# Kernel tuning notes

Measured on AMD Instinct MI355X. Metric: run time of the kernel, lower is better.

## Reference

```python
import jax, jax.numpy as jnp
import numpy as np
from jax.scipy.special import logsumexp

N_PROBLEMS = 10000
N_KCS = 100
N_STATES = 2
N_OUTPUTS = 2
BATCH = 1024
T = 500
TAU = 1.5


def setup_inputs() -> dict:
    key = jax.random.key(0)
    k1, k2, k3, k4, k5, k6, k7, k8 = jax.random.split(key, 8)
    corr = jax.random.randint(k1, (BATCH, T), 0, N_OUTPUTS)
    kc = jax.random.randint(k2, (BATCH, T), 0, N_PROBLEMS)
    problem = jax.random.randint(k3, (BATCH, T), 0, N_PROBLEMS)
    # learned parameters (per MultiHmmCell.__init__)
    trans_logits = jax.random.normal(k4, (N_KCS, N_STATES, N_STATES), dtype=jnp.float32)
    obs_logits_problem = 0.1 * jax.random.normal(k5, (N_PROBLEMS, N_STATES, N_OUTPUTS), dtype=jnp.float32)
    init_logits = jax.random.normal(k6, (N_KCS, N_STATES), dtype=jnp.float32)
    # BktModel.sample_A: gumbel-softmax over kc_membership_logits (soft, tau=1.5)
    kc_membership_logits = jax.random.normal(k7, (N_PROBLEMS, N_KCS), dtype=jnp.float32)
    u = jax.random.uniform(k8, (N_PROBLEMS, N_KCS), minval=1e-6, maxval=1.0 - 1e-6)
    gumbel = -jnp.log(-jnp.log(u))
    A = jax.nn.softmax((kc_membership_logits + gumbel) / TAU, axis=1)
    return {"corr": corr, "kc": kc, "problem": problem, "A": A,
            "trans_logits": trans_logits, "obs_logits_problem": obs_logits_problem,
            "init_logits": init_logits}


def _hmm_forward(corr, kc, problem, A, trans_logits, obs_logits_problem, init_logits):
    n_batch = corr.shape[0]
    chain = A[kc]                                           # [B, T, K] soft KC membership
    log_t = jax.nn.log_softmax(trans_logits, axis=1)        # [K, S, S] (normalized over dim 1, as in torch)
    log_alpha0 = jnp.broadcast_to(jax.nn.log_softmax(init_logits, axis=1)[None],
                                  (n_batch, init_logits.shape[0], init_logits.shape[1]))  # [B, K, S]

    def step(log_alpha, x):
        chain_t, prob_t, obs_t = x                          # [B,K], [B], [B]
        log_obs = jax.nn.log_softmax(obs_logits_problem[prob_t], axis=2)  # [B, S, O]
        # predicted output distribution
        a1 = log_obs * jnp.sum(chain_t, axis=1)[:, None, None]            # [B, S, O]
        a2 = jnp.einsum('bk,bks->bs', chain_t, log_alpha)                 # [B, S]
        log_py = logsumexp(a1 + a2[:, :, None], axis=1)                   # [B, O]
        log_py = log_py - logsumexp(log_py, axis=1, keepdims=True)
        # alpha update given observed output
        obs_ll = jnp.take_along_axis(log_obs, obs_t[:, None, None], axis=2)[:, :, 0]  # [B, S]
        obs_ll = obs_ll * jnp.sum(chain_t, axis=1)[:, None]
        a1b = jnp.einsum('bks,bk->bs', log_alpha, chain_t)                # [B, S]
        a2b = jnp.einsum('kso,bk->bso', log_t, chain_t)                   # [B, S, S]
        a3 = logsumexp(obs_ll[:, None, :] + a1b[:, None, :] + a2b, axis=2)  # [B, S]
        new_alpha = (1.0 - chain_t[:, :, None]) * log_alpha + chain_t[:, :, None] * a3[:, None, :]
        return new_alpha, log_py

    xs = (jnp.swapaxes(chain, 0, 1), problem.T, corr.T)
    _, outs = jax.lax.scan(step, log_alpha0, xs)            # outs: [T, B, O]
    return jnp.swapaxes(outs, 0, 1)                         # [B, T, O]


def reference(corr, kc, problem, A, trans_logits, obs_logits_problem, init_logits):
    return _hmm_forward(corr, kc, problem, A, trans_logits, obs_logits_problem, init_logits)
```

## Files before the change

### kernel.cpp

```cpp
#include <hip/hip_runtime.h>
#include <math.h>

#define B_  1024
#define T_  500
#define K_  100
#define NP_ 10000
#define CH  32
#define NCH 16

__device__ __forceinline__ float lse2(float a, float b) {
    float m = fmaxf(a, b);
    return m + __logf(__expf(a - m) + __expf(b - m));
}

template<int CTRL, int RM>
__device__ __forceinline__ float dpp_add(float v) {
    int x = __builtin_amdgcn_update_dpp(0, __float_as_int(v), CTRL, RM, 0xf, true);
    return v + __int_as_float(x);
}

__device__ __forceinline__ float wave_sum(float v) {
    v = dpp_add<0x111, 0xf>(v);
    v = dpp_add<0x112, 0xf>(v);
    v = dpp_add<0x114, 0xf>(v);
    v = dpp_add<0x118, 0xf>(v);
    v = dpp_add<0x142, 0xa>(v);
    v = dpp_add<0x143, 0xc>(v);
    return __int_as_float(__builtin_amdgcn_readlane(__float_as_int(v), 63));
}

#define GLOAD16(gp, lp) __builtin_amdgcn_global_load_lds( \
    (const __attribute__((address_space(1))) unsigned int*)(gp), \
    (__attribute__((address_space(3))) unsigned int*)(lp), 16, 0, 0)
#define GLOAD4(gp, lp) __builtin_amdgcn_global_load_lds( \
    (const __attribute__((address_space(1))) unsigned int*)(gp), \
    (__attribute__((address_space(3))) unsigned int*)(lp), 4, 0, 0)
#define WAITV0 asm volatile("s_waitcnt vmcnt(0)" ::: "memory")

__global__ __launch_bounds__(64, 4) void bkt_pre(
    const float* __restrict__ A, const float* __restrict__ trans,
    const float* __restrict__ obs, float* __restrict__ Qtab,
    float* __restrict__ Stab, float* __restrict__ LOtab)
{
    const int p = blockIdx.x;
    const int lane = threadIdx.x;
    const int k0 = lane, k1 = lane + 64;
    const bool has1 = (k1 < K_);
    const int k1c = has1 ? k1 : k0;
    const float m1 = has1 ? 1.f : 0.f;

    float4 t0 = *reinterpret_cast<const float4*>(trans + k0 * 4);
    float l00 = lse2(t0.x, t0.z), l01 = lse2(t0.y, t0.w);
    float lt000 = t0.x - l00, lt001 = t0.y - l01;
    float lt010 = t0.z - l00, lt011 = t0.w - l01;
    float4 t1 = *reinterpret_cast<const float4*>(trans + k1c * 4);
    float l10 = lse2(t1.x, t1.z), l11 = lse2(t1.y, t1.w);
    float lt100 = t1.x - l10, lt101 = t1.y - l11;
    float lt110 = t1.z - l10, lt111 = t1.w - l11;

    const float* ar = A + (size_t)p * K_;
    float c0 = ar[k0];
    float c1 = ar[k1c] * m1;

    float sc  = wave_sum(c0 + c1);
    float q00 = wave_sum(c0 * lt000 + c1 * lt100);
    float q01 = wave_sum(c0 * lt001 + c1 * lt101);
    float q10 = wave_sum(c0 * lt010 + c1 * lt110);
    float q11 = wave_sum(c0 * lt011 + c1 * lt111);

    float4 ob = *reinterpret_cast<const float4*>(obs + (size_t)p * 4);
    float l0 = lse2(ob.x, ob.y), l1 = lse2(ob.z, ob.w);

    if (lane == 0) {
        reinterpret_cast<float4*>(Qtab)[p] = make_float4(q00, q01, q10, q11);
        Stab[p] = sc;
        reinterpret_cast<float4*>(LOtab)[p] =
            make_float4(ob.x - l0, ob.y - l0, ob.z - l1, ob.w - l1);
    }
}

__global__ __launch_bounds__(64, 1) void bkt_main(
    const int* __restrict__ corr, const int* __restrict__ kc,
    const int* __restrict__ problem, const float* __restrict__ A,
    const float* __restrict__ init, const float* __restrict__ Qtab,
    const float* __restrict__ Stab, const float* __restrict__ LOtab,
    float* __restrict__ out)
{
    const int b = blockIdx.x;
    const int lane = threadIdx.x;
    const int k1 = lane + 64;
    const bool has1 = (k1 < K_);
    const int k1c = has1 ? k1 : lane;
    const float m1 = has1 ? 1.f : 0.f;

    __shared__ float  s_c[2][CH * K_];
    __shared__ float4 s_ql[2][2 * CH];
    __shared__ float  s_s[2][CH];
    __shared__ int    s_kcpr[3][2 * CH];
    __shared__ int    s_y[3][CH];
    __shared__ float2 s_a2[CH];

    const int* kcb = kc + (size_t)b * T_;
    const int* prb = problem + (size_t)b * T_;
    const int* cob = corr + (size_t)b * T_;
    float* outp = out + (size_t)b * T_ * 2;

    float al00, al01, al10 = 0.f, al11 = 0.f;
    {
        float2 x = *reinterpret_cast<const float2*>(init + lane * 2);
        float l = lse2(x.x, x.y);
        al00 = x.x - l; al01 = x.y - l;
    }
    {
        float2 x = *reinterpret_cast<const float2*>(init + k1c * 2);
        float l = lse2(x.x, x.y);
        al10 = (x.x - l) * m1; al11 = (x.y - l) * m1;
    }

#define STAGEIDX(cn, ib) {                                                \
        int tt_ = (cn) * CH + (lane & 31);                                \
        tt_ = tt_ < T_ ? tt_ : T_ - 1;                                    \
        const int* is_ = (lane < 32 ? kcb : prb) + tt_;                   \
        GLOAD4(is_, &s_kcpr[ib][0]);                                      \
        if (lane < 32) GLOAD4(cob + tt_, &s_y[ib][0]);                    \
    }

#define GATHER(ib, db) {                                                  \
        int myidx_ = s_kcpr[ib][lane];                                    \
        const float* qlsrc_ = (lane < 32)                                 \
            ? (Qtab  + (size_t)myidx_ * 4)                                \
            : (LOtab + (size_t)myidx_ * 4);                               \
        GLOAD16(qlsrc_, &s_ql[db][0]);                                    \
        if (lane < 32) GLOAD4(Stab + myidx_, &s_s[db][0]);                \
        _Pragma("unroll")                                                 \
        for (int j_ = 0; j_ < 13; ++j_) {                                 \
            int f_ = j_ * 64 + lane;                                      \
            unsigned tf_ = ((unsigned)f_ * 5243u) >> 17;        \
            int q_ = f_ - (int)tf_ * 25;                                  \
            int kcv_ = s_kcpr[ib][tf_];                                   \
            const float* asrc_ = A + (size_t)kcv_ * K_ + q_ * 4;          \
            if (f_ < CH * 25) GLOAD16(asrc_, &s_c[db][j_ * 256]);         \
        }                                                                 \
    }

    STAGEIDX(0, 0);
    STAGEIDX(1, 1);
    WAITV0;
    GATHER(0, 0);

#pragma unroll 1
    for (int n = 0; n < NCH; ++n) {
        WAITV0;
        { int i2 = (n + 2) % 3; STAGEIDX(n + 2, i2); }
        { int i1 = (n + 1) % 3, d1 = (n + 1) & 1; GATHER(i1, d1); }

        const float*  cbuf = s_c[n & 1];
        const float4* qlb  = s_ql[n & 1];
        const float*  sb   = s_s[n & 1];
        const int*    yb   = s_y[n % 3];
        const int base = n * CH;

        float ca0 = cbuf[lane];
        float ca1 = cbuf[k1c] * m1;
        float a20 = wave_sum(ca0 * al00 + ca1 * al10);
        float a21 = wave_sum(ca0 * al01 + ca1 * al11);

#pragma unroll 2
        for (int u = 0; u < CH - 1; ++u) {
            float cb0 = cbuf[(u + 1) * K_ + lane];
            float cb1 = cbuf[(u + 1) * K_ + k1c] * m1;
            float4 Q = qlb[u];
            float4 L = qlb[CH + u];
            float  S = sb[u];
            int    y = yb[u];
            if (lane == 0) s_a2[u] = make_float2(a20, a21);
            float hs0 = ((y == 0) ? L.x : L.y) * S;
            float hs1 = ((y == 0) ? L.z : L.w) * S;
            float a30 = lse2(hs0 + Q.x + a20, hs1 + Q.y + a21);
            float a31 = lse2(hs0 + Q.z + a20, hs1 + Q.w + a21);
            float tu0 = cb0 * (1.f - ca0), tu1 = cb1 * (1.f - ca1);
            float U0 = wave_sum(tu0 * al00 + tu1 * al10);
            float U1 = wave_sum(tu0 * al01 + tu1 * al11);
            float Wv = wave_sum(cb0 * ca0 + cb1 * ca1);
            al00 += ca0 * (a30 - al00);
            al01 += ca0 * (a31 - al01);
            al10 += ca1 * (a30 - al10);
            al11 += ca1 * (a31 - al11);
            a20 = U0 + Wv * a30;
            a21 = U1 + Wv * a31;
            ca0 = cb0; ca1 = cb1;
        }
        {
            const int u = CH - 1;
            float4 Q = qlb[u];
            float4 L = qlb[CH + u];
            float  S = sb[u];
            int    y = yb[u];
            if (lane == 0) s_a2[u] = make_float2(a20, a21);
            float hs0 = ((y == 0) ? L.x : L.y) * S;
            float hs1 = ((y == 0) ? L.z : L.w) * S;
            float a30 = lse2(hs0 + Q.x + a20, hs1 + Q.y + a21);
            float a31 = lse2(hs0 + Q.z + a20, hs1 + Q.w + a21);
            al00 += ca0 * (a30 - al00);
            al01 += ca0 * (a31 - al01);
            al10 += ca1 * (a30 - al10);
            al11 += ca1 * (a31 - al11);
        }
        if (lane < 32) {
            float2 a2v = s_a2[lane];
            float4 L = qlb[CH + lane];
            float  S = sb[lane];
            float h00 = L.x * S, h01 = L.y * S, h10 = L.z * S, h11 = L.w * S;
            float py0 = lse2(h00 + a2v.x, h10 + a2v.y);
            float py1 = lse2(h01 + a2v.x, h11 + a2v.y);
            float nrm = lse2(py0, py1);
            int t = base + lane;
            if (t < T_)
                *reinterpret_cast<float2*>(outp + (size_t)t * 2) =
                    make_float2(py0 - nrm, py1 - nrm);
        }
    }
#undef STAGEIDX
#undef GATHER
}

extern "C" void kernel_launch(void* const* d_in, const int* in_sizes, int n_in,
                              void* d_out, int out_size, void* d_ws, size_t ws_size,
                              hipStream_t stream) {
    const int*   corr    = (const int*)d_in[0];
    const int*   kc      = (const int*)d_in[1];
    const int*   problem = (const int*)d_in[2];
    const float* A       = (const float*)d_in[3];
    const float* trans   = (const float*)d_in[4];
    const float* obs     = (const float*)d_in[5];
    const float* init    = (const float*)d_in[6];
    float* out = (float*)d_out;

    float* Qtab  = (float*)d_ws;
    float* LOtab = Qtab + (size_t)NP_ * 4;
    float* Stab  = LOtab + (size_t)NP_ * 4;

    bkt_pre<<<NP_, 64, 0, stream>>>(A, trans, obs, Qtab, Stab, LOtab);
    bkt_main<<<B_, 64, 0, stream>>>(corr, kc, problem, A, init, Qtab, Stab, LOtab, out);
}
```

Before: 251.0 us.

## Precompute chunk-local alpha projections to shorten the serial recurrence chain

Restructures the per-timestep recurrence so that all wave reductions that do not depend on the serial a3 values are computed up front for a chunk of 8 steps. These are the pairwise coupling coefficients P[t][j] and the initial-alpha projections. The serial loop then needs only scalar FMAs and lse2 per step instead of three wave reductions. The cost is more total reductions (O(CH^2) per chunk), heavy register use for the P matrix, and smaller chunks with more pipeline iterations.

```diff
diff --git a/kernel.cpp b/kernel.cpp
--- a/kernel.cpp
+++ b/kernel.cpp
@@ -5,8 +5,8 @@
 #define T_  500
 #define K_  100
 #define NP_ 10000
-#define CH  32
-#define NCH 16
+#define CH  8
+#define NCH 64
 
 __device__ __forceinline__ float lse2(float a, float b) {
     float m = fmaxf(a, b);
@@ -96,9 +96,7 @@
     __shared__ float  s_c[2][CH * K_];
     __shared__ float4 s_ql[2][2 * CH];
     __shared__ float  s_s[2][CH];
-    __shared__ int    s_kcpr[3][2 * CH];
-    __shared__ int    s_y[3][CH];
-    __shared__ float2 s_a2[CH];
+    __shared__ int    s_idx[3][3 * CH];
 
     const int* kcb = kc + (size_t)b * T_;
     const int* prb = problem + (size_t)b * T_;
@@ -118,28 +116,27 @@
     }
 
 #define STAGEIDX(cn, ib) {                                                \
-        int tt_ = (cn) * CH + (lane & 31);                                \
+        int tt_ = (cn) * CH + (lane & 7);                                 \
         tt_ = tt_ < T_ ? tt_ : T_ - 1;                                    \
-        const int* is_ = (lane < 32 ? kcb : prb) + tt_;                   \
-        GLOAD4(is_, &s_kcpr[ib][0]);                                      \
-        if (lane < 32) GLOAD4(cob + tt_, &s_y[ib][0]);                    \
+        const int* src_ = (lane < 8) ? (kcb + tt_)                        \
+                        : (lane < 16) ? (prb + tt_) : (cob + tt_);        \
+        if (lane < 24) GLOAD4(src_, &s_idx[ib][0]);                       \
     }
 
 #define GATHER(ib, db) {                                                  \
-        int myidx_ = s_kcpr[ib][lane];                                    \
-        const float* qlsrc_ = (lane < 32)                                 \
-            ? (Qtab  + (size_t)myidx_ * 4)                                \
-            : (LOtab + (size_t)myidx_ * 4);                               \
-        GLOAD16(qlsrc_, &s_ql[db][0]);                                    \
-        if (lane < 32) GLOAD4(Stab + myidx_, &s_s[db][0]);                \
+        int id_ = s_idx[ib][lane & 15];                                   \
+        const float* qls_ = (lane < 8) ? (Qtab + (size_t)id_ * 4)         \
+                                       : (LOtab + (size_t)id_ * 4);       \
+        if (lane < 16) GLOAD16(qls_, &s_ql[db][0]);                       \
+        if (lane < 8)  GLOAD4(Stab + id_, &s_s[db][0]);                   \
         _Pragma("unroll")                                                 \
-        for (int j_ = 0; j_ < 13; ++j_) {                                 \
+        for (int j_ = 0; j_ < 4; ++j_) {                                  \
             int f_ = j_ * 64 + lane;                                      \
             unsigned tf_ = ((unsigned)f_ * 5243u) >> 17;        \
             int q_ = f_ - (int)tf_ * 25;                                  \
-            int kcv_ = s_kcpr[ib][tf_];                                   \
-            const float* asrc_ = A + (size_t)kcv_ * K_ + q_ * 4;          \
-            if (f_ < CH * 25) GLOAD16(asrc_, &s_c[db][j_ * 256]);         \
+            int kcv_ = s_idx[ib][tf_];                                    \
+            if (f_ < CH * 25)                                             \
+                GLOAD16(A + (size_t)kcv_ * K_ + q_ * 4, &s_c[db][j_ * 256]); \
         }                                                                 \
     }
 
@@ -151,70 +148,89 @@
 #pragma unroll 1
     for (int n = 0; n < NCH; ++n) {
         WAITV0;
-        { int i2 = (n + 2) % 3; STAGEIDX(n + 2, i2); }
-        { int i1 = (n + 1) % 3, d1 = (n + 1) & 1; GATHER(i1, d1); }
+        STAGEIDX(n + 2, (n + 2) % 3);
+        GATHER((n + 1) % 3, (n + 1) & 1);
 
         const float*  cbuf = s_c[n & 1];
         const float4* qlb  = s_ql[n & 1];
         const float*  sb   = s_s[n & 1];
-        const int*    yb   = s_y[n % 3];
-        const int base = n * CH;
-
-        float ca0 = cbuf[lane];
-        float ca1 = cbuf[k1c] * m1;
-        float a20 = wave_sum(ca0 * al00 + ca1 * al10);
-        float a21 = wave_sum(ca0 * al01 + ca1 * al11);
-
-#pragma unroll 2
-        for (int u = 0; u < CH - 1; ++u) {
-            float cb0 = cbuf[(u + 1) * K_ + lane];
-            float cb1 = cbuf[(u + 1) * K_ + k1c] * m1;
+        const int*    ibp  = s_idx[n % 3];
+
+        float c0r[CH], c1r[CH], d0r[CH], d1r[CH];
+#pragma unroll
+        for (int u = 0; u < CH; ++u) {
+            c0r[u] = cbuf[u * K_ + lane];
+            c1r[u] = cbuf[u * K_ + k1c] * m1;
+        }
+#pragma unroll
+        for (int u = 0; u < CH; ++u) {
+            d0r[u] = 1.f - c0r[u];
+            d1r[u] = 1.f - c1r[u];
+        }
+
+        float g0[CH], g1[CH], g2[CH], g3[CH];
+#pragma unroll
+        for (int u = 0; u < CH; ++u) {
             float4 Q = qlb[u];
             float4 L = qlb[CH + u];
             float  S = sb[u];
-            int    y = yb[u];
-            if (lane == 0) s_a2[u] = make_float2(a20, a21);
+            int    y = ibp[16 + u];
             float hs0 = ((y == 0) ? L.x : L.y) * S;
             float hs1 = ((y == 0) ? L.z : L.w) * S;
-            float a30 = lse2(hs0 + Q.x + a20, hs1 + Q.y + a21);
-            float a31 = lse2(hs0 + Q.z + a20, hs1 + Q.w + a21);
-            float tu0 = cb0 * (1.f - ca0), tu1 = cb1 * (1.f - ca1);
-            float U0 = wave_sum(tu0 * al00 + tu1 * al10);
-            float U1 = wave_sum(tu0 * al01 + tu1 * al11);
-            float Wv = wave_sum(cb0 * ca0 + cb1 * ca1);
-            al00 += ca0 * (a30 - al00);
-            al01 += ca0 * (a31 - al01);
-            al10 += ca1 * (a30 - al10);
-            al11 += ca1 * (a31 - al11);
-            a20 = U0 + Wv * a30;
-            a21 = U1 + Wv * a31;
-            ca0 = cb0; ca1 = cb1;
-        }
+            g0[u] = hs0 + Q.x; g1[u] = hs1 + Q.y;
+            g2[u] = hs0 + Q.z; g3[u] = hs1 + Q.w;
+        }
+
+        float P[CH][CH];
+#pragma unroll
+        for (int j = 0; j < CH - 1; ++j) {
+            float v0 = c0r[j], v1 = c1r[j];
+#pragma unroll
+            for (int t = j + 1; t < CH; ++t) {
+                P[t][j] = wave_sum(c0r[t] * v0 + c1r[t] * v1);
+                v0 *= d0r[t]; v1 *= d1r[t];
+            }
+        }
+
+        float a2acc0[CH], a2acc1[CH];
         {
-            const int u = CH - 1;
-            float4 Q = qlb[u];
-            float4 L = qlb[CH + u];
-            float  S = sb[u];
-            int    y = yb[u];
-            if (lane == 0) s_a2[u] = make_float2(a20, a21);
-            float hs0 = ((y == 0) ? L.x : L.y) * S;
-            float hs1 = ((y == 0) ? L.z : L.w) * S;
-            float a30 = lse2(hs0 + Q.x + a20, hs1 + Q.y + a21);
-            float a31 = lse2(hs0 + Q.z + a20, hs1 + Q.w + a21);
-            al00 += ca0 * (a30 - al00);
-            al01 += ca0 * (a31 - al01);
-            al10 += ca1 * (a30 - al10);
-            al11 += ca1 * (a31 - al11);
-        }
-        if (lane < 32) {
-            float2 a2v = s_a2[lane];
+            float w00 = al00, w01 = al01, w10 = al10, w11 = al11;
+#pragma unroll
+            for (int u = 0; u < CH; ++u) {
+                a2acc0[u] = wave_sum(c0r[u] * w00 + c1r[u] * w10);
+                a2acc1[u] = wave_sum(c0r[u] * w01 + c1r[u] * w11);
+                w00 *= d0r[u]; w01 *= d0r[u];
+                w10 *= d1r[u]; w11 *= d1r[u];
+            }
+        }
+
+        float keep0 = 0.f, keep1 = 0.f;
+#pragma unroll
+        for (int u = 0; u < CH; ++u) {
+            float a20 = a2acc0[u], a21 = a2acc1[u];
+            keep0 = (lane == u) ? a20 : keep0;
+            keep1 = (lane == u) ? a21 : keep1;
+            float a30 = lse2(g0[u] + a20, g1[u] + a21);
+            float a31 = lse2(g2[u] + a20, g3[u] + a21);
+#pragma unroll
+            for (int v = u + 1; v < CH; ++v) {
+                a2acc0[v] += P[v][u] * a30;
+                a2acc1[v] += P[v][u] * a31;
+            }
+            al00 += c0r[u] * (a30 - al00);
+            al01 += c0r[u] * (a31 - al01);
+            al10 += c1r[u] * (a30 - al10);
+            al11 += c1r[u] * (a31 - al11);
+        }
+
+        if (lane < CH) {
             float4 L = qlb[CH + lane];
             float  S = sb[lane];
             float h00 = L.x * S, h01 = L.y * S, h10 = L.z * S, h11 = L.w * S;
-            float py0 = lse2(h00 + a2v.x, h10 + a2v.y);
-            float py1 = lse2(h01 + a2v.x, h11 + a2v.y);
+            float py0 = lse2(h00 + keep0, h10 + keep1);
+            float py1 = lse2(h01 + keep0, h11 + keep1);
             float nrm = lse2(py0, py1);
-            int t = base + lane;
+            int t = n * CH + lane;
             if (t < T_)
                 *reinterpret_cast<float2*>(outp + (size_t)t * 2) =
                     make_float2(py0 - nrm, py1 - nrm);
```

New measurement: 372.0 us. +48.2%, slower.
